# Optimization experiments

Measured on AMD Instinct MI355X. Metric: run time of the kernel, lower is better.

The kernel has to match this reference:

```python
import jax, jax.numpy as jnp
import numpy as np

D_MODEL = 1024
NUM_HEADS = 16
HEAD_DIM = D_MODEL // NUM_HEADS


def setup_inputs() -> dict:
    key = jax.random.key(0)
    ks = jax.random.split(key, 5)
    B, S = 4, 2048
    x = jax.random.normal(ks[0], (B, S, D_MODEL), dtype=jnp.float32)
    scale = 1.0 / np.sqrt(D_MODEL)
    qkv_w = jax.random.normal(ks[1], (3 * D_MODEL, D_MODEL), dtype=jnp.float32) * scale
    qkv_b = jnp.zeros((3 * D_MODEL,), dtype=jnp.float32)
    out_w = jax.random.normal(ks[2], (D_MODEL, D_MODEL), dtype=jnp.float32) * scale
    out_b = jnp.zeros((D_MODEL,), dtype=jnp.float32)
    return {"x": x, "qkv_w": qkv_w, "qkv_b": qkv_b, "out_w": out_w, "out_b": out_b}


def reference(x, qkv_w, qkv_b, out_w, out_b):
    B, S, _ = x.shape
    # qkv projection (torch Linear: x @ W.T + b)
    qkv = x @ qkv_w.T + qkv_b  # [B, S, 3*D]
    q, k, v = jnp.split(qkv, 3, axis=-1)
    # [B, H, S, hd]
    q = q.reshape(B, S, NUM_HEADS, HEAD_DIM).transpose(0, 2, 1, 3)
    k = k.reshape(B, S, NUM_HEADS, HEAD_DIM).transpose(0, 2, 1, 3)
    v = v.reshape(B, S, NUM_HEADS, HEAD_DIM).transpose(0, 2, 1, 3)
    scores = jnp.einsum('bhqd,bhkd->bhqk', q, k) / np.sqrt(HEAD_DIM).astype(np.float32)
    attn = jax.nn.softmax(scores, axis=-1)
    context = jnp.einsum('bhqk,bhkd->bhqd', attn, v)  # [B, H, S, hd]
    context = context.transpose(0, 2, 1, 3).reshape(B, S, D_MODEL)
    return context @ out_w.T + out_b
```

## Files before the change

### kernel.cpp

```cpp
#include <hip/hip_runtime.h>
#include <hip/hip_bf16.h>
#include <math.h>

#define D_MODEL 1024
#define NHEADS  16
#define HDIM    64
#define BATCH   4
#define SLEN    2048
#define MROWS   (BATCH * SLEN)
#define QKV_N   (3 * D_MODEL)

typedef __attribute__((ext_vector_type(8))) short bhalf8;
typedef __attribute__((ext_vector_type(4))) float f32x4;

#if __has_builtin(__builtin_amdgcn_exp2f)
#define EXP2(x) __builtin_amdgcn_exp2f(x)
#else
#define EXP2(x) exp2f(x)
#endif

static __device__ __forceinline__ unsigned short f2bf(float f) {
    unsigned int u = __builtin_bit_cast(unsigned int, f);
    unsigned int r = (u + 0x7FFFu + ((u >> 16) & 1u)) >> 16;
    return (unsigned short)r;
}

static __device__ __forceinline__ unsigned int pack_hi16(float lo, float hi) {
    return __builtin_amdgcn_perm(__builtin_bit_cast(unsigned int, hi),
                                 __builtin_bit_cast(unsigned int, lo),
                                 0x07060302u);
}

static __device__ __forceinline__ void load_lds16(const void* g, void* l) {
    __builtin_amdgcn_global_load_lds(
        (const __attribute__((address_space(1))) void*)g,
        (__attribute__((address_space(3))) void*)l, 16, 0, 0);
}

__global__ __launch_bounds__(256) void cast_f32_bf16(
    const float* __restrict__ in, unsigned short* __restrict__ out, int n)
{
    int i = (blockIdx.x * 256 + threadIdx.x) * 4;
    if (i < n) {
        float4 v = *(const float4*)(in + i);
        ushort4 o;
        o.x = f2bf(v.x); o.y = f2bf(v.y); o.z = f2bf(v.z); o.w = f2bf(v.w);
        *(ushort4*)(out + i) = o;
    }
}

template<bool BF16OUT>
__global__ __launch_bounds__(256) void gemm_mfma_bt(
    const unsigned short* __restrict__ A,
    const unsigned short* __restrict__ W,
    const float* __restrict__ bias,
    void* __restrict__ outv,
    int M, int N, int K, int qcols, float qscale)
{
    __shared__ __align__(16) unsigned short As[128 * 32];
    __shared__ __align__(16) unsigned short Bs[128 * 32];

    const int tid  = threadIdx.x;
    const int bm   = blockIdx.y * 128;
    const int bn   = blockIdx.x * 128;
    const int wave = tid >> 6;
    const int lane = tid & 63;
    const int m16  = lane & 15;
    const int quad = lane >> 4;
    const int wm   = (wave & 1) * 64;
    const int wn   = (wave >> 1) * 64;

    const int r0 = tid >> 2;
    const int s0 = tid & 3;
    const int g0 = (s0 - (r0 >> 1)) & 3;
    const int g1 = (s0 - ((r0 + 64) >> 1)) & 3;

    const size_t arow0 = (size_t)(bm + r0) * K + g0 * 8;
    const size_t arow1 = (size_t)(bm + r0 + 64) * K + g1 * 8;
    const size_t brow0 = (size_t)(bn + r0) * K + g0 * 8;
    const size_t brow1 = (size_t)(bn + r0 + 64) * K + g1 * 8;

    f32x4 acc[4][4];
    f32x4 zero = {0.f, 0.f, 0.f, 0.f};
#pragma unroll
    for (int i = 0; i < 4; ++i)
#pragma unroll
        for (int j = 0; j < 4; ++j) acc[i][j] = zero;

    for (int kt = 0; kt < K; kt += 32) {
        __syncthreads();
        load_lds16(A + arow0 + kt, As + tid * 8);
        load_lds16(A + arow1 + kt, As + 2048 + tid * 8);
        load_lds16(W + brow0 + kt, Bs + tid * 8);
        load_lds16(W + brow1 + kt, Bs + 2048 + tid * 8);
        __asm__ volatile("s_waitcnt vmcnt(0)" ::: "memory");
        __syncthreads();

        bhalf8 af[4], bf[4];
#pragma unroll
        for (int i = 0; i < 4; ++i) {
            int ra = wm + i * 16 + m16;
            int sa = (quad + (ra >> 1)) & 3;
            af[i] = *(const bhalf8*)&As[ra * 32 + sa * 8];
        }
#pragma unroll
        for (int j = 0; j < 4; ++j) {
            int rb = wn + j * 16 + m16;
            int sb = (quad + (rb >> 1)) & 3;
            bf[j] = *(const bhalf8*)&Bs[rb * 32 + sb * 8];
        }
#pragma unroll
        for (int i = 0; i < 4; ++i)
#pragma unroll
            for (int j = 0; j < 4; ++j)
                acc[i][j] = __builtin_amdgcn_mfma_f32_16x16x32_bf16(
                    af[i], bf[j], acc[i][j], 0, 0, 0);
    }

    float bj[4], scj[4];
#pragma unroll
    for (int j = 0; j < 4; ++j) {
        int col = bn + wn + j * 16 + m16;
        bj[j]  = bias[col];
        scj[j] = (col < qcols) ? qscale : 1.0f;
    }

#pragma unroll
    for (int i = 0; i < 4; ++i) {
#pragma unroll
        for (int r = 0; r < 4; ++r) {
            size_t row = (size_t)(bm + wm + i * 16 + quad * 4 + r);
            if (BF16OUT) {
                unsigned short* dst = (unsigned short*)outv + row * N + bn + wn;
#pragma unroll
                for (int j = 0; j < 4; ++j)
                    dst[j * 16 + m16] = f2bf((acc[i][j][r] + bj[j]) * scj[j]);
            } else {
                float* dst = (float*)outv + row * N + bn + wn;
#pragma unroll
                for (int j = 0; j < 4; ++j)
                    dst[j * 16 + m16] = (acc[i][j][r] + bj[j]) * scj[j];
            }
        }
    }
}

__global__ __launch_bounds__(256, 4) void attn_mfma_kernel(
    const unsigned short* __restrict__ qkv, unsigned short* __restrict__ ctx)
{
    const int qt = blockIdx.x;
    const int h  = blockIdx.y;
    const int b  = blockIdx.z;
    const int tid  = threadIdx.x;
    const int wave = tid >> 6;
    const int lane = tid & 63;
    const int m16  = lane & 15;
    const int quad = lane >> 4;

    __shared__ __align__(16) unsigned short K_lds[64 * 64];
    __shared__ __align__(16) unsigned short Vt_lds[64 * 72];
    __shared__ __align__(16) unsigned short QP_lds[4 * 32 * 72];

    const int srow  = tid >> 3;
    const int sslot = tid & 7;

    {
        const unsigned short* qbase =
            qkv + (size_t)(b * SLEN + qt * 128) * QKV_N + h * HDIM;
#pragma unroll
        for (int c = 0; c < 4; ++c) {
            int r = c * 32 + srow;
            int g = (sslot - r) & 7;
            load_lds16(qbase + (size_t)r * QKV_N + g * 8,
                       QP_lds + c * 2048 + tid * 8);
        }
    }
    __asm__ volatile("s_waitcnt vmcnt(0)" ::: "memory");
    __syncthreads();

    bhalf8 qf[2][2];
#pragma unroll
    for (int qi = 0; qi < 2; ++qi) {
        int rq = wave * 32 + qi * 16 + m16;
#pragma unroll
        for (int ks = 0; ks < 2; ++ks) {
            int slot = (ks * 4 + quad + rq) & 7;
            qf[qi][ks] = *(const bhalf8*)&QP_lds[rq * 64 + slot * 8];
        }
    }

    f32x4 zero = {0.f, 0.f, 0.f, 0.f};
    f32x4 oacc[2][4], oacc_l[2];
#pragma unroll
    for (int qi = 0; qi < 2; ++qi) {
        oacc_l[qi] = zero;
#pragma unroll
        for (int dt = 0; dt < 4; ++dt) oacc[qi][dt] = zero;
    }

    bhalf8 ones;
#pragma unroll
    for (int i = 0; i < 8; ++i) ones[i] = (short)0x3F80;

    const int u    = tid & 31;
    const int k0   = (u & 15) | ((u & 16) << 1);
    const int idx0 = (u & 15) * 4 + ((u >> 4) << 1);
    const int vd0  = (tid >> 5) * 8;

    unsigned short* P = &QP_lds[wave * (32 * 72)];

    for (int kt = 0; kt < SLEN / 64; ++kt) {
        __syncthreads();

        {
            const unsigned short* kbase =
                qkv + (size_t)(b * SLEN + kt * 64) * QKV_N + D_MODEL + h * HDIM;
#pragma unroll
            for (int c = 0; c < 2; ++c) {
                int r = c * 32 + srow;
                int g = (sslot - r) & 7;
                load_lds16(kbase + (size_t)r * QKV_N + g * 8,
                           K_lds + c * 2048 + tid * 8);
            }
        }
        {
            const unsigned short* vbase =
                qkv + (size_t)(b * SLEN + kt * 64) * QKV_N + 2 * D_MODEL + h * HDIM;
            uint4 va = *(const uint4*)(vbase + (size_t)k0 * QKV_N + vd0);
            uint4 vb = *(const uint4*)(vbase + (size_t)(k0 + 16) * QKV_N + vd0);
            unsigned int* dst0 = (unsigned int*)&Vt_lds[(vd0 + 0) * 72 + idx0];
            unsigned int* dst1 = (unsigned int*)&Vt_lds[(vd0 + 1) * 72 + idx0];
            dst0[0]            = __builtin_amdgcn_perm(vb.x, va.x, 0x05040100u);
            dst1[0]            = __builtin_amdgcn_perm(vb.x, va.x, 0x07060302u);
            *(unsigned int*)&Vt_lds[(vd0 + 2) * 72 + idx0] = __builtin_amdgcn_perm(vb.y, va.y, 0x05040100u);
            *(unsigned int*)&Vt_lds[(vd0 + 3) * 72 + idx0] = __builtin_amdgcn_perm(vb.y, va.y, 0x07060302u);
            *(unsigned int*)&Vt_lds[(vd0 + 4) * 72 + idx0] = __builtin_amdgcn_perm(vb.z, va.z, 0x05040100u);
            *(unsigned int*)&Vt_lds[(vd0 + 5) * 72 + idx0] = __builtin_amdgcn_perm(vb.z, va.z, 0x07060302u);
            *(unsigned int*)&Vt_lds[(vd0 + 6) * 72 + idx0] = __builtin_amdgcn_perm(vb.w, va.w, 0x05040100u);
            *(unsigned int*)&Vt_lds[(vd0 + 7) * 72 + idx0] = __builtin_amdgcn_perm(vb.w, va.w, 0x07060302u);
        }
        __asm__ volatile("s_waitcnt vmcnt(0)" ::: "memory");
        __syncthreads();

        f32x4 sacc[2][4];
#pragma unroll
        for (int qi = 0; qi < 2; ++qi)
#pragma unroll
            for (int nt = 0; nt < 4; ++nt) sacc[qi][nt] = zero;
#pragma unroll
        for (int ks = 0; ks < 2; ++ks) {
#pragma unroll
            for (int nt = 0; nt < 4; ++nt) {
                int rk = nt * 16 + m16;
                int slot = (ks * 4 + quad + rk) & 7;
                bhalf8 kf = *(const bhalf8*)&K_lds[rk * 64 + slot * 8];
                sacc[0][nt] = __builtin_amdgcn_mfma_f32_16x16x32_bf16(
                    qf[0][ks], kf, sacc[0][nt], 0, 0, 0);
                sacc[1][nt] = __builtin_amdgcn_mfma_f32_16x16x32_bf16(
                    qf[1][ks], kf, sacc[1][nt], 0, 0, 0);
            }
        }

#pragma unroll
        for (int qi = 0; qi < 2; ++qi) {
#pragma unroll
            for (int r = 0; r < 4; ++r) {
                float p0 = EXP2(sacc[qi][0][r]);
                float p1 = EXP2(sacc[qi][1][r]);
                float p2 = EXP2(sacc[qi][2][r]);
                float p3 = EXP2(sacc[qi][3][r]);
                uint2 w;
                w.x = pack_hi16(p0, p1);
                w.y = pack_hi16(p2, p3);
                *(uint2*)&P[(qi * 16 + quad * 4 + r) * 72 + m16 * 4] = w;
            }
        }

        __asm__ volatile("s_waitcnt lgkmcnt(0)" ::: "memory");

#pragma unroll
        for (int ks = 0; ks < 2; ++ks) {
            bhalf8 pf0 = *(const bhalf8*)&P[(m16)      * 72 + ks * 32 + quad * 8];
            bhalf8 pf1 = *(const bhalf8*)&P[(16 + m16) * 72 + ks * 32 + quad * 8];
            oacc_l[0] = __builtin_amdgcn_mfma_f32_16x16x32_bf16(pf0, ones, oacc_l[0], 0, 0, 0);
            oacc_l[1] = __builtin_amdgcn_mfma_f32_16x16x32_bf16(pf1, ones, oacc_l[1], 0, 0, 0);
#pragma unroll
            for (int dt = 0; dt < 4; ++dt) {
                bhalf8 vf = *(const bhalf8*)&Vt_lds[(dt * 16 + m16) * 72 + ks * 32 + quad * 8];
                oacc[0][dt] = __builtin_amdgcn_mfma_f32_16x16x32_bf16(pf0, vf, oacc[0][dt], 0, 0, 0);
                oacc[1][dt] = __builtin_amdgcn_mfma_f32_16x16x32_bf16(pf1, vf, oacc[1][dt], 0, 0, 0);
            }
        }
    }

#pragma unroll
    for (int qi = 0; qi < 2; ++qi) {
#pragma unroll
        for (int r = 0; r < 4; ++r) {
            float inv = 1.0f / oacc_l[qi][r];
            int row = b * SLEN + qt * 128 + wave * 32 + qi * 16 + quad * 4 + r;
            unsigned short* dst = ctx + (size_t)row * D_MODEL + h * HDIM;
#pragma unroll
            for (int dt = 0; dt < 4; ++dt)
                dst[dt * 16 + m16] = f2bf(oacc[qi][dt][r] * inv);
        }
    }
}

extern "C" void kernel_launch(void* const* d_in, const int* in_sizes, int n_in,
                              void* d_out, int out_size, void* d_ws, size_t ws_size,
                              hipStream_t stream)
{
    const float* x     = (const float*)d_in[0];
    const float* qkv_w = (const float*)d_in[1];
    const float* qkv_b = (const float*)d_in[2];
    const float* out_w = (const float*)d_in[3];
    const float* out_b = (const float*)d_in[4];
    float* out = (float*)d_out;

    unsigned short* xbf  = (unsigned short*)d_ws;
    unsigned short* wqkv = xbf  + (size_t)MROWS * D_MODEL;
    unsigned short* wout = wqkv + (size_t)QKV_N * D_MODEL;
    unsigned short* qkv  = wout + (size_t)D_MODEL * D_MODEL;
    unsigned short* ctx  = qkv  + (size_t)MROWS * QKV_N;

    {
        int n;
        n = MROWS * D_MODEL;
        cast_f32_bf16<<<n / 1024, 256, 0, stream>>>(x, xbf, n);
        n = QKV_N * D_MODEL;
        cast_f32_bf16<<<n / 1024, 256, 0, stream>>>(qkv_w, wqkv, n);
        n = D_MODEL * D_MODEL;
        cast_f32_bf16<<<n / 1024, 256, 0, stream>>>(out_w, wout, n);
    }

    const float QSCALE = 0.125f * 1.44269504088896f;

    {
        dim3 grid(QKV_N / 128, MROWS / 128);
        gemm_mfma_bt<true><<<grid, 256, 0, stream>>>(xbf, wqkv, qkv_b, qkv,
                                                     MROWS, QKV_N, D_MODEL,
                                                     D_MODEL, QSCALE);
    }

    {
        dim3 grid(SLEN / 128, NHEADS, BATCH);
        attn_mfma_kernel<<<grid, 256, 0, stream>>>(qkv, ctx);
    }

    {
        dim3 grid(D_MODEL / 128, MROWS / 128);
        gemm_mfma_bt<false><<<grid, 256, 0, stream>>>(ctx, wout, out_b, out,
                                                      MROWS, D_MODEL, D_MODEL,
                                                      0, 1.0f);
    }
}
```

Measured before the change: 289.0 us.

## Use 256x256 triple-buffered MFMA GEMM for QKV projection

```diff
diff --git a/kernel.cpp b/kernel.cpp
--- a/kernel.cpp
+++ b/kernel.cpp
@@ -46,6 +46,124 @@
         ushort4 o;
         o.x = f2bf(v.x); o.y = f2bf(v.y); o.z = f2bf(v.z); o.w = f2bf(v.w);
         *(ushort4*)(out + i) = o;
+    }
+}
+
+template<bool BF16OUT>
+__global__ __launch_bounds__(512, 2) void gemm256_mfma_bt(
+    const unsigned short* __restrict__ A,
+    const unsigned short* __restrict__ W,
+    const float* __restrict__ bias,
+    void* __restrict__ outv,
+    int M, int N, int K, int qcols, float qscale)
+{
+    __shared__ __align__(16) unsigned short As[3][256 * 32];
+    __shared__ __align__(16) unsigned short Bs[3][256 * 32];
+
+    const int tid  = threadIdx.x;
+    const int bm   = blockIdx.y * 256;
+    const int bn   = blockIdx.x * 256;
+    const int wave = tid >> 6;
+    const int lane = tid & 63;
+    const int m16  = lane & 15;
+    const int quad = lane >> 4;
+    const int wm   = (wave >> 2) * 128;
+    const int wn   = (wave & 3) * 64;
+
+    const int r0 = tid >> 2;
+    const int s0 = tid & 3;
+    const int g0 = (s0 - (r0 >> 1)) & 3;
+
+    const size_t arow0 = (size_t)(bm + r0)       * K + g0 * 8;
+    const size_t arow1 = (size_t)(bm + r0 + 128) * K + g0 * 8;
+    const size_t brow0 = (size_t)(bn + r0)       * K + g0 * 8;
+    const size_t brow1 = (size_t)(bn + r0 + 128) * K + g0 * 8;
+
+    f32x4 acc[8][4];
+    f32x4 zero = {0.f, 0.f, 0.f, 0.f};
+#pragma unroll
+    for (int i = 0; i < 8; ++i)
+#pragma unroll
+        for (int j = 0; j < 4; ++j) acc[i][j] = zero;
+
+    const int NT = K >> 5;
+
+#define STAGE256(tile, slot) do {                                        \
+        int koff_ = (tile) << 5;                                         \
+        load_lds16(A + arow0 + koff_, &As[slot][tid * 8]);               \
+        load_lds16(A + arow1 + koff_, &As[slot][4096 + tid * 8]);        \
+        load_lds16(W + brow0 + koff_, &Bs[slot][tid * 8]);               \
+        load_lds16(W + brow1 + koff_, &Bs[slot][4096 + tid * 8]);        \
+    } while (0)
+
+    STAGE256(0, 0);
+    STAGE256(1, 1);
+
+    int cs = 0, ss = 2;
+    for (int t = 0; t < NT; ++t) {
+        if (t < NT - 1)
+            __asm__ volatile("s_waitcnt vmcnt(4)" ::: "memory");
+        else
+            __asm__ volatile("s_waitcnt vmcnt(0)" ::: "memory");
+        __builtin_amdgcn_s_barrier();
+        __asm__ volatile("" ::: "memory");
+
+        if (t + 2 < NT) STAGE256(t + 2, ss);
+
+        const unsigned short* Ab = &As[cs][0];
+        const unsigned short* Bb = &Bs[cs][0];
+        bhalf8 af[8], bq[4];
+#pragma unroll
+        for (int i = 0; i < 8; ++i) {
+            int ra = wm + i * 16 + m16;
+            int sa = (quad + (ra >> 1)) & 3;
+            af[i] = *(const bhalf8*)&Ab[ra * 32 + sa * 8];
+        }
+#pragma unroll
+        for (int j = 0; j < 4; ++j) {
+            int rb = wn + j * 16 + m16;
+            int sb = (quad + (rb >> 1)) & 3;
+            bq[j] = *(const bhalf8*)&Bb[rb * 32 + sb * 8];
+        }
+        __builtin_amdgcn_s_setprio(1);
+#pragma unroll
+        for (int i = 0; i < 8; ++i)
+#pragma unroll
+            for (int j = 0; j < 4; ++j)
+                acc[i][j] = __builtin_amdgcn_mfma_f32_16x16x32_bf16(
+                    af[i], bq[j], acc[i][j], 0, 0, 0);
+        __builtin_amdgcn_s_setprio(0);
+
+        cs = cs == 2 ? 0 : cs + 1;
+        ss = ss == 2 ? 0 : ss + 1;
+    }
+#undef STAGE256
+
+    float bj[4], scj[4];
+#pragma unroll
+    for (int j = 0; j < 4; ++j) {
+        int col = bn + wn + j * 16 + m16;
+        bj[j]  = bias[col];
+        scj[j] = (col < qcols) ? qscale : 1.0f;
+    }
+
+#pragma unroll
+    for (int i = 0; i < 8; ++i) {
+#pragma unroll
+        for (int r = 0; r < 4; ++r) {
+            size_t row = (size_t)(bm + wm + i * 16 + quad * 4 + r);
+            if (BF16OUT) {
+                unsigned short* dst = (unsigned short*)outv + row * N + bn + wn;
+#pragma unroll
+                for (int j = 0; j < 4; ++j)
+                    dst[j * 16 + m16] = f2bf((acc[i][j][r] + bj[j]) * scj[j]);
+            } else {
+                float* dst = (float*)outv + row * N + bn + wn;
+#pragma unroll
+                for (int j = 0; j < 4; ++j)
+                    dst[j * 16 + m16] = (acc[i][j][r] + bj[j]) * scj[j];
+            }
+        }
     }
 }
 
@@ -337,10 +455,10 @@
     const float QSCALE = 0.125f * 1.44269504088896f;
 
     {
-        dim3 grid(QKV_N / 128, MROWS / 128);
-        gemm_mfma_bt<true><<<grid, 256, 0, stream>>>(xbf, wqkv, qkv_b, qkv,
-                                                     MROWS, QKV_N, D_MODEL,
-                                                     D_MODEL, QSCALE);
+        dim3 grid(QKV_N / 256, MROWS / 256);
+        gemm256_mfma_bt<true><<<grid, 512, 0, stream>>>(xbf, wqkv, qkv_b, qkv,
+                                                        MROWS, QKV_N, D_MODEL,
+                                                        D_MODEL, QSCALE);
     }
 
     {
```

New measurement: 296.0 us. +2.4%, slower.

## Software-pipeline K/V tile loads in attention kernel and remap block order

Applied to the files above, without the earlier changes.

```diff
diff --git a/kernel.cpp b/kernel.cpp
--- a/kernel.cpp
+++ b/kernel.cpp
@@ -19,6 +19,8 @@
 #define EXP2(x) exp2f(x)
 #endif
 
+#define MFMA16(a, b, c) __builtin_amdgcn_mfma_f32_16x16x32_bf16((a), (b), (c), 0, 0, 0)
+
 static __device__ __forceinline__ unsigned short f2bf(float f) {
     unsigned int u = __builtin_bit_cast(unsigned int, f);
     unsigned int r = (u + 0x7FFFu + ((u >> 16) & 1u)) >> 16;
@@ -36,6 +38,14 @@
         (const __attribute__((address_space(1))) void*)g,
         (__attribute__((address_space(3))) void*)l, 16, 0, 0);
 }
+
+#define FENCE() __asm__ volatile("" ::: "memory")
+#define BARRIER() do { FENCE();                                   \
+        __builtin_amdgcn_sched_barrier(0);                        \
+        __builtin_amdgcn_s_barrier();                             \
+        __builtin_amdgcn_sched_barrier(0); FENCE(); } while (0)
+#define WAIT_VM(N)   __asm__ volatile("s_waitcnt vmcnt(" #N ")" ::: "memory")
+#define WAIT_LGKM0() __asm__ volatile("s_waitcnt lgkmcnt(0)" ::: "memory")
 
 __global__ __launch_bounds__(256) void cast_f32_bf16(
     const float* __restrict__ in, unsigned short* __restrict__ out, int n)
@@ -148,9 +158,12 @@
 __global__ __launch_bounds__(256, 4) void attn_mfma_kernel(
     const unsigned short* __restrict__ qkv, unsigned short* __restrict__ ctx)
 {
-    const int qt = blockIdx.x;
-    const int h  = blockIdx.y;
-    const int b  = blockIdx.z;
+    const int orig = blockIdx.x + (blockIdx.y << 4) + (blockIdx.z << 8);
+    const int flat = ((orig & 7) << 7) | (orig >> 3);
+    const int qt = flat & 15;
+    const int h  = (flat >> 4) & 15;
+    const int b  = flat >> 8;
+
     const int tid  = threadIdx.x;
     const int wave = tid >> 6;
     const int lane = tid & 63;
@@ -163,6 +176,44 @@
 
     const int srow  = tid >> 3;
     const int sslot = tid & 7;
+    const int gk    = (sslot - srow) & 7;
+
+    const int u    = tid & 31;
+    const int k0   = (u & 15) | ((u & 16) << 1);
+    const int idx0 = (u & 15) * 4 + ((u >> 4) << 1);
+    const int vd0  = (tid >> 5) * 8;
+
+    const unsigned short* kPtr =
+        qkv + ((size_t)b * SLEN) * QKV_N + D_MODEL + h * HDIM
+            + (size_t)srow * QKV_N + gk * 8;
+    const unsigned short* vPtr0 =
+        qkv + ((size_t)b * SLEN) * QKV_N + 2 * D_MODEL + h * HDIM
+            + (size_t)k0 * QKV_N + vd0;
+    const unsigned short* vPtr1 = vPtr0 + (size_t)16 * QKV_N;
+
+    uint4 va_A, vb_A, va_B, vb_B;
+
+#define ISSUE_K(T) do {                                                      \
+        const unsigned short* kb_ = kPtr + (size_t)(T) * 64 * QKV_N;         \
+        load_lds16(kb_,                        K_lds + tid * 8);             \
+        load_lds16(kb_ + (size_t)32 * QKV_N,   K_lds + 2048 + tid * 8);      \
+    } while (0)
+
+#define ISSUE_V(T, VA, VB) do {                                              \
+        VA = *(const uint4*)(vPtr0 + (size_t)(T) * 64 * QKV_N);              \
+        VB = *(const uint4*)(vPtr1 + (size_t)(T) * 64 * QKV_N);              \
+    } while (0)
+
+#define WRITE_V(VA, VB) do {                                                                         \
+        *(unsigned int*)&Vt_lds[(vd0 + 0) * 72 + idx0] = __builtin_amdgcn_perm(VB.x, VA.x, 0x05040100u); \
+        *(unsigned int*)&Vt_lds[(vd0 + 1) * 72 + idx0] = __builtin_amdgcn_perm(VB.x, VA.x, 0x07060302u); \
+        *(unsigned int*)&Vt_lds[(vd0 + 2) * 72 + idx0] = __builtin_amdgcn_perm(VB.y, VA.y, 0x05040100u); \
+        *(unsigned int*)&Vt_lds[(vd0 + 3) * 72 + idx0] = __builtin_amdgcn_perm(VB.y, VA.y, 0x07060302u); \
+        *(unsigned int*)&Vt_lds[(vd0 + 4) * 72 + idx0] = __builtin_amdgcn_perm(VB.z, VA.z, 0x05040100u); \
+        *(unsigned int*)&Vt_lds[(vd0 + 5) * 72 + idx0] = __builtin_amdgcn_perm(VB.z, VA.z, 0x07060302u); \
+        *(unsigned int*)&Vt_lds[(vd0 + 6) * 72 + idx0] = __builtin_amdgcn_perm(VB.w, VA.w, 0x05040100u); \
+        *(unsigned int*)&Vt_lds[(vd0 + 7) * 72 + idx0] = __builtin_amdgcn_perm(VB.w, VA.w, 0x07060302u); \
+    } while (0)
 
     {
         const unsigned short* qbase =
@@ -175,8 +226,10 @@
                        QP_lds + c * 2048 + tid * 8);
         }
     }
-    __asm__ volatile("s_waitcnt vmcnt(0)" ::: "memory");
-    __syncthreads();
+    ISSUE_K(0);
+    ISSUE_V(0, va_A, vb_A);
+    WAIT_VM(2);
+    BARRIER();
 
     bhalf8 qf[2][2];
 #pragma unroll
@@ -189,6 +242,12 @@
         }
     }
 
+    WAIT_VM(0);
+    WRITE_V(va_A, vb_A);
+    ISSUE_V(1, va_B, vb_B);
+    WAIT_LGKM0();
+    BARRIER();
+
     f32x4 zero = {0.f, 0.f, 0.f, 0.f};
     f32x4 oacc[2][4], oacc_l[2];
 #pragma unroll
@@ -202,96 +261,109 @@
 #pragma unroll
     for (int i = 0; i < 8; ++i) ones[i] = (short)0x3F80;
 
-    const int u    = tid & 31;
-    const int k0   = (u & 15) | ((u & 16) << 1);
-    const int idx0 = (u & 15) * 4 + ((u >> 4) << 1);
-    const int vd0  = (tid >> 5) * 8;
-
     unsigned short* P = &QP_lds[wave * (32 * 72)];
-
-    for (int kt = 0; kt < SLEN / 64; ++kt) {
-        __syncthreads();
-
-        {
-            const unsigned short* kbase =
-                qkv + (size_t)(b * SLEN + kt * 64) * QKV_N + D_MODEL + h * HDIM;
-#pragma unroll
-            for (int c = 0; c < 2; ++c) {
-                int r = c * 32 + srow;
-                int g = (sslot - r) & 7;
-                load_lds16(kbase + (size_t)r * QKV_N + g * 8,
-                           K_lds + c * 2048 + tid * 8);
-            }
-        }
-        {
-            const unsigned short* vbase =
-                qkv + (size_t)(b * SLEN + kt * 64) * QKV_N + 2 * D_MODEL + h * HDIM;
-            uint4 va = *(const uint4*)(vbase + (size_t)k0 * QKV_N + vd0);
-            uint4 vb = *(const uint4*)(vbase + (size_t)(k0 + 16) * QKV_N + vd0);
-            unsigned int* dst0 = (unsigned int*)&Vt_lds[(vd0 + 0) * 72 + idx0];
-            unsigned int* dst1 = (unsigned int*)&Vt_lds[(vd0 + 1) * 72 + idx0];
-            dst0[0]            = __builtin_amdgcn_perm(vb.x, va.x, 0x05040100u);
-            dst1[0]            = __builtin_amdgcn_perm(vb.x, va.x, 0x07060302u);
-            *(unsigned int*)&Vt_lds[(vd0 + 2) * 72 + idx0] = __builtin_amdgcn_perm(vb.y, va.y, 0x05040100u);
-            *(unsigned int*)&Vt_lds[(vd0 + 3) * 72 + idx0] = __builtin_amdgcn_perm(vb.y, va.y, 0x07060302u);
-            *(unsigned int*)&Vt_lds[(vd0 + 4) * 72 + idx0] = __builtin_amdgcn_perm(vb.z, va.z, 0x05040100u);
-            *(unsigned int*)&Vt_lds[(vd0 + 5) * 72 + idx0] = __builtin_amdgcn_perm(vb.z, va.z, 0x07060302u);
-            *(unsigned int*)&Vt_lds[(vd0 + 6) * 72 + idx0] = __builtin_amdgcn_perm(vb.w, va.w, 0x05040100u);
-            *(unsigned int*)&Vt_lds[(vd0 + 7) * 72 + idx0] = __builtin_amdgcn_perm(vb.w, va.w, 0x07060302u);
-        }
-        __asm__ volatile("s_waitcnt vmcnt(0)" ::: "memory");
-        __syncthreads();
-
-        f32x4 sacc[2][4];
-#pragma unroll
-        for (int qi = 0; qi < 2; ++qi)
-#pragma unroll
-            for (int nt = 0; nt < 4; ++nt) sacc[qi][nt] = zero;
-#pragma unroll
-        for (int ks = 0; ks < 2; ++ks) {
-#pragma unroll
-            for (int nt = 0; nt < 4; ++nt) {
-                int rk = nt * 16 + m16;
-                int slot = (ks * 4 + quad + rk) & 7;
-                bhalf8 kf = *(const bhalf8*)&K_lds[rk * 64 + slot * 8];
-                sacc[0][nt] = __builtin_amdgcn_mfma_f32_16x16x32_bf16(
-                    qf[0][ks], kf, sacc[0][nt], 0, 0, 0);
-                sacc[1][nt] = __builtin_amdgcn_mfma_f32_16x16x32_bf16(
-                    qf[1][ks], kf, sacc[1][nt], 0, 0, 0);
-            }
-        }
-
-#pragma unroll
-        for (int qi = 0; qi < 2; ++qi) {
-#pragma unroll
-            for (int r = 0; r < 4; ++r) {
-                float p0 = EXP2(sacc[qi][0][r]);
-                float p1 = EXP2(sacc[qi][1][r]);
-                float p2 = EXP2(sacc[qi][2][r]);
-                float p3 = EXP2(sacc[qi][3][r]);
-                uint2 w;
-                w.x = pack_hi16(p0, p1);
-                w.y = pack_hi16(p2, p3);
-                *(uint2*)&P[(qi * 16 + quad * 4 + r) * 72 + m16 * 4] = w;
-            }
-        }
-
-        __asm__ volatile("s_waitcnt lgkmcnt(0)" ::: "memory");
-
-#pragma unroll
-        for (int ks = 0; ks < 2; ++ks) {
-            bhalf8 pf0 = *(const bhalf8*)&P[(m16)      * 72 + ks * 32 + quad * 8];
-            bhalf8 pf1 = *(const bhalf8*)&P[(16 + m16) * 72 + ks * 32 + quad * 8];
-            oacc_l[0] = __builtin_amdgcn_mfma_f32_16x16x32_bf16(pf0, ones, oacc_l[0], 0, 0, 0);
-            oacc_l[1] = __builtin_amdgcn_mfma_f32_16x16x32_bf16(pf1, ones, oacc_l[1], 0, 0, 0);
-#pragma unroll
-            for (int dt = 0; dt < 4; ++dt) {
-                bhalf8 vf = *(const bhalf8*)&Vt_lds[(dt * 16 + m16) * 72 + ks * 32 + quad * 8];
-                oacc[0][dt] = __builtin_amdgcn_mfma_f32_16x16x32_bf16(pf0, vf, oacc[0][dt], 0, 0, 0);
-                oacc[1][dt] = __builtin_amdgcn_mfma_f32_16x16x32_bf16(pf1, vf, oacc[1][dt], 0, 0, 0);
-            }
-        }
-    }
+    f32x4 sacc[2][4];
+
+#define QKT_PHASE() do {                                                     \
+        _Pragma("unroll")                                                    \
+        for (int qi = 0; qi < 2; ++qi)                                       \
+            _Pragma("unroll")                                                \
+            for (int nt = 0; nt < 4; ++nt) sacc[qi][nt] = zero;              \
+        __builtin_amdgcn_s_setprio(1);                                       \
+        _Pragma("unroll")                                                    \
+        for (int ks = 0; ks < 2; ++ks) {                                     \
+            _Pragma("unroll")                                                \
+            for (int nt = 0; nt < 4; ++nt) {                                 \
+                int rk = nt * 16 + m16;                                      \
+                int slot = (ks * 4 + quad + rk) & 7;                         \
+                bhalf8 kf = *(const bhalf8*)&K_lds[rk * 64 + slot * 8];      \
+                sacc[0][nt] = MFMA16(qf[0][ks], kf, sacc[0][nt]);            \
+                sacc[1][nt] = MFMA16(qf[1][ks], kf, sacc[1][nt]);            \
+            }                                                                \
+        }                                                                    \
+        __builtin_amdgcn_s_setprio(0);                                       \
+    } while (0)
+
+#define SOFTMAX_PHASE() do {                                                 \
+        _Pragma("unroll")                                                    \
+        for (int qi = 0; qi < 2; ++qi) {                                     \
+            _Pragma("unroll")                                                \
+            for (int r = 0; r < 4; ++r) {                                    \
+                float p0 = EXP2(sacc[qi][0][r]);                             \
+                float p1 = EXP2(sacc[qi][1][r]);                             \
+                float p2 = EXP2(sacc[qi][2][r]);                             \
+                float p3 = EXP2(sacc[qi][3][r]);                             \
+                uint2 w;                                                     \
+                w.x = pack_hi16(p0, p1);                                     \
+                w.y = pack_hi16(p2, p3);                                     \
+                *(uint2*)&P[(qi * 16 + quad * 4 + r) * 72 + m16 * 4] = w;    \
+            }                                                                \
+        }                                                                    \
+        WAIT_LGKM0();                                                        \
+        __builtin_amdgcn_sched_barrier(0);                                   \
+    } while (0)
+
+#define PV_PHASE() do {                                                      \
+        __builtin_amdgcn_s_setprio(1);                                       \
+        _Pragma("unroll")                                                    \
+        for (int ks = 0; ks < 2; ++ks) {                                     \
+            bhalf8 pf0 = *(const bhalf8*)&P[(m16)      * 72 + ks * 32 + quad * 8]; \
+            bhalf8 pf1 = *(const bhalf8*)&P[(16 + m16) * 72 + ks * 32 + quad * 8]; \
+            oacc_l[0] = MFMA16(pf0, ones, oacc_l[0]);                        \
+            oacc_l[1] = MFMA16(pf1, ones, oacc_l[1]);                        \
+            _Pragma("unroll")                                                \
+            for (int dt = 0; dt < 4; ++dt) {                                 \
+                bhalf8 vf = *(const bhalf8*)&Vt_lds[(dt * 16 + m16) * 72 + ks * 32 + quad * 8]; \
+                oacc[0][dt] = MFMA16(pf0, vf, oacc[0][dt]);                  \
+                oacc[1][dt] = MFMA16(pf1, vf, oacc[1][dt]);                  \
+            }                                                                \
+        }                                                                    \
+        __builtin_amdgcn_s_setprio(0);                                       \
+    } while (0)
+
+#define TILE_FULL(T, VAW, VBW, VAL, VBL) do {                                \
+        QKT_PHASE();                                                         \
+        BARRIER();                     \
+        ISSUE_K((T) + 1);                                                    \
+        SOFTMAX_PHASE();                                                     \
+        PV_PHASE();                                                          \
+        BARRIER();                     \
+        WAIT_VM(2);                    \
+        WRITE_V(VAW, VBW);                                                   \
+        ISSUE_V((T) + 2, VAL, VBL);                                          \
+        WAIT_VM(2);                    \
+        WAIT_LGKM0();                                                        \
+        BARRIER();                     \
+    } while (0)
+
+    for (int t2 = 0; t2 < 30; t2 += 2) {
+        TILE_FULL(t2,     va_B, vb_B, va_A, vb_A);
+        TILE_FULL(t2 + 1, va_A, vb_A, va_B, vb_B);
+    }
+
+    QKT_PHASE();
+    BARRIER();
+    ISSUE_K(31);
+    SOFTMAX_PHASE();
+    PV_PHASE();
+    BARRIER();
+    WAIT_VM(2);
+    WRITE_V(va_B, vb_B);
+    WAIT_VM(0);
+    WAIT_LGKM0();
+    BARRIER();
+
+    QKT_PHASE();
+    SOFTMAX_PHASE();
+    PV_PHASE();
+
+#undef TILE_FULL
+#undef PV_PHASE
+#undef SOFTMAX_PHASE
+#undef QKT_PHASE
+#undef WRITE_V
+#undef ISSUE_V
+#undef ISSUE_K
 
 #pragma unroll
     for (int qi = 0; qi < 2; ++qi) {
```

After: 280.7 us. 2.9% less time.
